# Optimization experiments

Measured on AMD Instinct MI355X. Metric: run time of the kernel, lower is better.

## Reference

```python
import jax, jax.numpy as jnp
import numpy as np

H = 2048      # hidden_size
I = 8192      # dense intermediate_size
MI = 1024     # moe_intermediate_size
E = 8         # num_local_experts
K = 2         # num_experts_per_tok
B, S = 2, 1024
EPS = 1e-6
ROOT = H ** (-0.5)


def _rms(x, w=None, eps=EPS):
    # fp32 RMSNorm matching _Gemma4CPURMSNorm; w=None -> no-scale variant
    ms = jnp.mean(x * x, axis=-1, keepdims=True) + eps
    y = x * jax.lax.rsqrt(ms)
    return y * w if w is not None else y


def _gelu_tanh(x):
    # gelu_pytorch_tanh == tanh-approximate gelu
    return jax.nn.gelu(x, approximate=True)


def setup_inputs() -> dict:
    key = jax.random.key(0)
    ks = jax.random.split(key, 10)
    s = 0.02
    return {
        "hidden_states": jax.random.normal(ks[0], (B, S, H), jnp.float32),
        # RMSNorm scales (init ones, as in nn.Parameter(torch.ones(dim)))
        "rn_pre1": jnp.ones((H,), jnp.float32),
        "rn_pre2": jnp.ones((H,), jnp.float32),
        "rn_post1": jnp.ones((H,), jnp.float32),
        "rn_post2": jnp.ones((H,), jnp.float32),
        "rn_post": jnp.ones((H,), jnp.float32),
        # dense GLU MLP weights, stored (in, out)
        "w_gate": jax.random.normal(ks[1], (H, I), jnp.float32) * s,
        "w_up":   jax.random.normal(ks[2], (H, I), jnp.float32) * s,
        "w_down": jax.random.normal(ks[3], (I, H), jnp.float32) * s,
        # router
        "router_w": jax.random.normal(ks[4], (H, E), jnp.float32) * s,
        "router_scale": jnp.ones((H,), jnp.float32),
        "per_expert_scale": jnp.ones((E,), jnp.float32),
        # per-expert GLU weights, stacked over experts
        "we_gate": jax.random.normal(ks[5], (E, H, MI), jnp.float32) * s,
        "we_up":   jax.random.normal(ks[6], (E, H, MI), jnp.float32) * s,
        "we_down": jax.random.normal(ks[7], (E, MI, H), jnp.float32) * s,
    }


def reference(hidden_states, rn_pre1, rn_pre2, rn_post1, rn_post2, rn_post,
              w_gate, w_up, w_down, router_w, router_scale, per_expert_scale,
              we_gate, we_up, we_down):
    b, s, h = hidden_states.shape
    T = b * s

    # --- dense branch ---
    dense_in = _rms(hidden_states, rn_pre1)                      # (B,S,H)
    dense_out = (_gelu_tanh(dense_in @ w_gate) * (dense_in @ w_up)) @ w_down
    dense_out = _rms(dense_out, rn_post1)                        # (B,S,H)

    # --- router (takes the raw residual, applies its own no-scale RMSNorm) ---
    x = hidden_states.reshape(T, h)
    xr = _rms(x) * router_scale * ROOT                           # (T,H)
    router_logits = xr @ router_w                                # (T,E)
    probs = jax.nn.softmax(router_logits, axis=-1)
    top_w, top_i = jax.lax.top_k(probs, K)                       # (T,K)
    top_w = top_w / jnp.sum(top_w, axis=-1, keepdims=True)
    top_w = top_w * per_expert_scale[top_i]
    aff = jnp.zeros((T, E), x.dtype).at[jnp.arange(T)[:, None], top_i].set(top_w)

    # --- MoE experts (compute all experts, combine with sparse affinities) ---
    moe_in = _rms(hidden_states, rn_pre2).reshape(T, h)          # (T,H)
    g = jnp.einsum('th,ehm->tem', moe_in, we_gate)               # (T,E,MI)
    u = jnp.einsum('th,ehm->tem', moe_in, we_up)
    eo = jnp.einsum('tem,emh->teh', _gelu_tanh(g) * u, we_down)  # (T,E,H)
    moe_out = jnp.einsum('te,teh->th', aff, eo).reshape(b, s, h)
    moe_out = _rms(moe_out, rn_post2)

    return _rms(dense_out + moe_out, rn_post)
```

## Files before the change

### kernel.cpp

```cpp
#include <hip/hip_runtime.h>
#include <stdint.h>

#define TOK 2048
#define HD  2048
#define ID  8192
#define MID 1024
#define NE  8
#define KSPLIT 4

typedef __attribute__((ext_vector_type(8))) short s16x8;
typedef __attribute__((ext_vector_type(4))) short s16x4;
typedef __attribute__((ext_vector_type(4))) float f32x4;

constexpr float EPSF  = 1e-6f;
constexpr float ROOTF = 0.02209708691207961f;

#define MFMA(a, b, c) __builtin_amdgcn_mfma_f32_16x16x32_bf16(a, b, c, 0, 0, 0)
#define BAR() __builtin_amdgcn_s_barrier()
#define SCHED0() __builtin_amdgcn_sched_barrier(0)
#define VMCNT(n) asm volatile("s_waitcnt vmcnt(" #n ")" ::: "memory")

__device__ __forceinline__ void gload16(const void* g, void* l) {
  __builtin_amdgcn_global_load_lds(
      (const __attribute__((address_space(1))) void*)g,
      (__attribute__((address_space(3))) void*)l, 16, 0, 0);
}

__device__ __forceinline__ short f2bf(float f) {
  union { float f; uint32_t u; } v; v.f = f;
  uint32_t r = v.u + 0x7fffu + ((v.u >> 16) & 1u);
  return (short)(r >> 16);
}

__device__ __forceinline__ float bf2f(short s) {
  union { uint32_t u; float f; } v; v.u = ((uint32_t)(uint16_t)s) << 16;
  return v.f;
}

__device__ __forceinline__ float gelu_tanh(float x) {
  float x3 = x * x * x;
  float u = 0.7978845608028654f * (x + 0.044715f * x3);
  return 0.5f * x * (1.0f + tanhf(u));
}

__global__ __launch_bounds__(256) void k_rms_router(
    const float* __restrict__ x, const float* __restrict__ rnp1,
    const float* __restrict__ rnp2, const float* __restrict__ rsc,
    const float* __restrict__ rw, const float* __restrict__ pes,
    short* __restrict__ rms1, short* __restrict__ rms2,
    int* __restrict__ cnt, int* __restrict__ tokl,
    float* __restrict__ wgtl, int* __restrict__ slotl) {
  const int t = blockIdx.x, tid = threadIdx.x;
  const size_t base = (size_t)t * HD;
  f32x4 v[2];
  float ss = 0.f;
#pragma unroll
  for (int i = 0; i < 2; ++i) {
    v[i] = *(const f32x4*)(x + base + tid * 4 + i * 1024);
#pragma unroll
    for (int j = 0; j < 4; ++j) ss += v[i][j] * v[i][j];
  }
  __shared__ float sr[4];
  __shared__ float sl[32];
#pragma unroll
  for (int off = 32; off; off >>= 1) ss += __shfl_down(ss, off, 64);
  if ((tid & 63) == 0) sr[tid >> 6] = ss;
  __syncthreads();
  const float inv = rsqrtf((sr[0] + sr[1] + sr[2] + sr[3]) * (1.0f / HD) + EPSF);
  float p[8] = {0, 0, 0, 0, 0, 0, 0, 0};
#pragma unroll
  for (int i = 0; i < 2; ++i) {
    const int h = tid * 4 + i * 1024;
    f32x4 w1 = *(const f32x4*)(rnp1 + h);
    f32x4 w2 = *(const f32x4*)(rnp2 + h);
    f32x4 sc = *(const f32x4*)(rsc + h);
    s16x4 o1, o2;
#pragma unroll
    for (int j = 0; j < 4; ++j) {
      float xn = v[i][j] * inv;
      o1[j] = f2bf(xn * w1[j]);
      o2[j] = f2bf(xn * w2[j]);
      float xq = xn * sc[j] * ROOTF;
      const float* rr = rw + (size_t)(h + j) * NE;
      f32x4 ra = *(const f32x4*)rr;
      f32x4 rb = *(const f32x4*)(rr + 4);
      p[0] += xq * ra[0]; p[1] += xq * ra[1]; p[2] += xq * ra[2]; p[3] += xq * ra[3];
      p[4] += xq * rb[0]; p[5] += xq * rb[1]; p[6] += xq * rb[2]; p[7] += xq * rb[3];
    }
    *(s16x4*)(rms1 + base + h) = o1;
    *(s16x4*)(rms2 + base + h) = o2;
  }
#pragma unroll
  for (int e = 0; e < 8; ++e)
#pragma unroll
    for (int off = 32; off; off >>= 1) p[e] += __shfl_down(p[e], off, 64);
  if ((tid & 63) == 0) {
#pragma unroll
    for (int e = 0; e < 8; ++e) sl[(tid >> 6) * 8 + e] = p[e];
  }
  __syncthreads();
  if (tid == 0) {
    float l[8];
#pragma unroll
    for (int e = 0; e < 8; ++e) l[e] = sl[e] + sl[8 + e] + sl[16 + e] + sl[24 + e];
    int i1 = 0;
#pragma unroll
    for (int e = 1; e < 8; ++e) if (l[e] > l[i1]) i1 = e;
    int i2 = (i1 == 0) ? 1 : 0;
#pragma unroll
    for (int e = 0; e < 8; ++e) if (e != i1 && l[e] > l[i2]) i2 = e;
    float p2 = expf(l[i2] - l[i1]);
    float s = 1.0f + p2;
    float w1 = (1.0f / s) * pes[i1];
    float w2 = (p2 / s) * pes[i2];
    int q1 = atomicAdd(&cnt[i1], 1);
    tokl[i1 * TOK + q1] = t; wgtl[i1 * TOK + q1] = w1; slotl[i1 * TOK + q1] = 0;
    int q2 = atomicAdd(&cnt[i2], 1);
    tokl[i2 * TOK + q2] = t; wgtl[i2 * TOK + q2] = w2; slotl[i2 * TOK + q2] = 1;
  }
}

__global__ __launch_bounds__(256) void k_transpose(
    const float* __restrict__ in, short* __restrict__ out, int R, int C) {
  __shared__ float tile[64 * 65];
  const int tid = threadIdx.x;
  const int c0 = blockIdx.x * 64, r0 = blockIdx.y * 64;
  const size_t bo = (size_t)blockIdx.z * R * C;
#pragma unroll
  for (int i = 0; i < 4; ++i) {
    int idx = tid + 256 * i;
    int r = idx >> 4, c4 = idx & 15;
    f32x4 f = *(const f32x4*)(in + bo + (size_t)(r0 + r) * C + c0 + c4 * 4);
#pragma unroll
    for (int j = 0; j < 4; ++j) tile[(c4 * 4 + j) * 65 + r] = f[j];
  }
  __syncthreads();
#pragma unroll
  for (int i = 0; i < 2; ++i) {
    int ch = tid + 256 * i;
    int c = ch >> 3, rs = ch & 7;
    s16x8 o;
#pragma unroll
    for (int q = 0; q < 8; ++q) o[q] = f2bf(tile[c * 65 + rs * 8 + q]);
    *(s16x8*)(out + bo + (size_t)(c0 + c) * R + r0 + rs * 8) = o;
  }
}

__global__ __launch_bounds__(512, 2) void k_gemm256(
    const short* __restrict__ Wt,
    const short* __restrict__ X,
    short* __restrict__ C) {
  __shared__ char lds[2][65536];
  const int tid = threadIdx.x;
  const int lane = tid & 63, wave = tid >> 6;
  const int wr = wave >> 2, wc = wave & 3;
  const int ln15 = lane & 15, l16 = lane >> 4;
  const int m0 = blockIdx.x * 256, t0 = blockIdx.y * 256;
  const int swz = (ln15 & 7) << 4;
  const int srow = tid >> 3;
  const int sslot = ((tid & 7) ^ ((tid >> 3) & 7)) << 4;
  const char* Wb = (const char*)Wt;
  const char* Xb = (const char*)X;
  auto STAGE = [&](int kt, int s) {
#pragma unroll
    for (int c = 0; c < 4; ++c) {
      gload16(Wb + (size_t)(m0 + c * 64 + srow) * 4096 + kt * 128 + sslot,
              &lds[s][c * 8192] + wave * 1024);
      gload16(Xb + (size_t)(t0 + c * 64 + srow) * 4096 + kt * 128 + sslot,
              &lds[s][32768 + c * 8192] + wave * 1024);
    }
  };
  f32x4 acc[8][4];
#pragma unroll
  for (int m = 0; m < 8; ++m)
#pragma unroll
    for (int n = 0; n < 4; ++n) acc[m][n] = (f32x4)0.f;
  const int NT = HD / 64;
  STAGE(0, 0);
  STAGE(1, 1);
  VMCNT(8);
  SCHED0();
  BAR();
#pragma unroll 2
  for (int kt = 0; kt < NT; ++kt) {
    const int s = kt & 1;
    const char* sA = &lds[s][0];
    const char* sB = &lds[s][32768];
#pragma unroll
    for (int mh = 0; mh < 2; ++mh)
#pragma unroll
      for (int ks = 0; ks < 2; ++ks) {
        const int ka = (ks * 64 + l16 * 16) ^ swz;
        s16x8 a[4], b[4];
#pragma unroll
        for (int f = 0; f < 4; ++f)
          a[f] = *(const s16x8*)(sA + (wr * 128 + mh * 64 + f * 16 + ln15) * 128 + ka);
#pragma unroll
        for (int n = 0; n < 4; ++n)
          b[n] = *(const s16x8*)(sB + (wc * 64 + n * 16 + ln15) * 128 + ka);
        __builtin_amdgcn_s_setprio(1);
#pragma unroll
        for (int f = 0; f < 4; ++f)
#pragma unroll
          for (int n = 0; n < 4; ++n)
            acc[mh * 4 + f][n] = MFMA(a[f], b[n], acc[mh * 4 + f][n]);
        __builtin_amdgcn_s_setprio(0);
      }
    BAR();
    if (kt + 2 < NT) {
      STAGE(kt + 2, s);
      VMCNT(8);
    } else if (kt + 1 < NT) {
      VMCNT(0);
    }
    SCHED0();
    BAR();
  }
#pragma unroll
  for (int mi = 0; mi < 8; ++mi)
#pragma unroll
    for (int n = 0; n < 4; ++n) {
      const int t = t0 + wc * 64 + n * 16 + ln15;
      const int i = m0 + wr * 128 + mi * 16 + l16 * 4;
      s16x4 o;
#pragma unroll
      for (int r = 0; r < 4; ++r) o[r] = f2bf(acc[mi][n][r]);
      *(s16x4*)(C + (size_t)t * ID + i) = o;
    }
}

__global__ __launch_bounds__(256) void k_gelumul(
    const short* __restrict__ g, const short* __restrict__ u,
    short* __restrict__ o) {
  const size_t idx = ((size_t)blockIdx.x * 256 + threadIdx.x) * 8;
  s16x8 gv = *(const s16x8*)(g + idx);
  s16x8 uv = *(const s16x8*)(u + idx);
  s16x8 ov;
#pragma unroll
  for (int j = 0; j < 8; ++j)
    ov[j] = f2bf(gelu_tanh(bf2f(gv[j])) * bf2f(uv[j]));
  *(s16x8*)(o + idx) = ov;
}

__global__ __launch_bounds__(256) void k_dense_down(
    const short* __restrict__ wdT,
    const short* __restrict__ act,
    float* __restrict__ dparts) {
  __shared__ short sW[128 * 32];
  __shared__ short sX[128 * 32];
  const int tid = threadIdx.x;
  const int n0 = blockIdx.x * 128, t0 = blockIdx.y * 128;
  const int kbase = blockIdx.z * (ID / KSPLIT);
  const int lane = tid & 63, wave = tid >> 6;
  const int wr = wave >> 1, wc = wave & 1;
  const int ln15 = lane & 15, k8 = (lane >> 4) * 8;
  const int srow = tid >> 2, skc = (tid & 3) * 8;
  const short* gW0 = wdT + (size_t)(n0 + srow) * ID + kbase + skc;
  const short* gW1 = wdT + (size_t)(n0 + 64 + srow) * ID + kbase + skc;
  const short* gX0 = act + (size_t)(t0 + srow) * ID + kbase + skc;
  const short* gX1 = act + (size_t)(t0 + 64 + srow) * ID + kbase + skc;
  char* lW = (char*)sW + wave * 1024;
  char* lX = (char*)sX + wave * 1024;
  f32x4 acc[4][4];
#pragma unroll
  for (int m = 0; m < 4; ++m)
#pragma unroll
    for (int n = 0; n < 4; ++n) acc[m][n] = (f32x4)0.f;
  for (int kt = 0; kt < ID / KSPLIT / 32; ++kt) {
    const int ko = kt * 32;
    __syncthreads();
    gload16(gW0 + ko, lW);
    gload16(gW1 + ko, lW + 4096);
    gload16(gX0 + ko, lX);
    gload16(gX1 + ko, lX + 4096);
    __syncthreads();
    s16x8 a[4], b[4];
#pragma unroll
    for (int m = 0; m < 4; ++m)
      a[m] = *(const s16x8*)(sW + (wr * 64 + m * 16 + ln15) * 32 + k8);
#pragma unroll
    for (int n = 0; n < 4; ++n)
      b[n] = *(const s16x8*)(sX + (wc * 64 + n * 16 + ln15) * 32 + k8);
#pragma unroll
    for (int m = 0; m < 4; ++m)
#pragma unroll
      for (int n = 0; n < 4; ++n) acc[m][n] = MFMA(a[m], b[n], acc[m][n]);
  }
  float* dst = dparts + (size_t)blockIdx.z * TOK * HD;
#pragma unroll
  for (int n = 0; n < 4; ++n) {
    const int t = t0 + wc * 64 + n * 16 + ln15;
#pragma unroll
    for (int m = 0; m < 4; ++m) {
      const int h = n0 + wr * 64 + m * 16 + (lane >> 4) * 4;
      *(f32x4*)(dst + (size_t)t * HD + h) = acc[m][n];
    }
  }
}

__global__ __launch_bounds__(256) void k_exp_gateup(
    const short* __restrict__ wegT, const short* __restrict__ weuT,
    const short* __restrict__ rms2,
    const int* __restrict__ cnt, const int* __restrict__ tokl,
    short* __restrict__ acte) {
  const int e = blockIdx.z;
  const int cn = cnt[e];
  const int t0 = blockIdx.y * 128;
  if (t0 >= cn) return;
  const int n0 = blockIdx.x * 64;
  __shared__ short sW[128 * 32];
  __shared__ short sX[128 * 32];
  const int tid = threadIdx.x;
  const int lane = tid & 63, wave = tid >> 6;
  const int ln15 = lane & 15, k8 = (lane >> 4) * 8;
  const int nsub = (wave & 1) * 32, tsub = (wave >> 1) * 64;
  const int srow = tid >> 2, skc = (tid & 3) * 8;
  const int* tl = tokl + e * TOK;
  int r0 = t0 + srow, r1 = t0 + 64 + srow;
  int tk0 = tl[r0 < cn ? r0 : cn - 1];
  int tk1 = tl[r1 < cn ? r1 : cn - 1];
  const short* gW0 = wegT + (size_t)e * MID * HD + (size_t)(n0 + srow) * HD + skc;
  const short* gW1 = weuT + (size_t)e * MID * HD + (size_t)(n0 + srow) * HD + skc;
  const short* gX0 = rms2 + (size_t)tk0 * HD + skc;
  const short* gX1 = rms2 + (size_t)tk1 * HD + skc;
  char* lW = (char*)sW + wave * 1024;
  char* lX = (char*)sX + wave * 1024;
  f32x4 accg[2][4], accu[2][4];
#pragma unroll
  for (int m = 0; m < 2; ++m)
#pragma unroll
    for (int n = 0; n < 4; ++n) { accg[m][n] = (f32x4)0.f; accu[m][n] = (f32x4)0.f; }
  for (int kt = 0; kt < HD / 32; ++kt) {
    const int ko = kt * 32;
    __syncthreads();
    gload16(gW0 + ko, lW);
    gload16(gW1 + ko, lW + 4096);
    gload16(gX0 + ko, lX);
    gload16(gX1 + ko, lX + 4096);
    __syncthreads();
    s16x8 ag[2], au[2], bx[4];
#pragma unroll
    for (int m = 0; m < 2; ++m) {
      ag[m] = *(const s16x8*)(sW + (nsub + m * 16 + ln15) * 32 + k8);
      au[m] = *(const s16x8*)(sW + (64 + nsub + m * 16 + ln15) * 32 + k8);
    }
#pragma unroll
    for (int n = 0; n < 4; ++n)
      bx[n] = *(const s16x8*)(sX + (tsub + n * 16 + ln15) * 32 + k8);
#pragma unroll
    for (int m = 0; m < 2; ++m)
#pragma unroll
      for (int n = 0; n < 4; ++n) {
        accg[m][n] = MFMA(ag[m], bx[n], accg[m][n]);
        accu[m][n] = MFMA(au[m], bx[n], accu[m][n]);
      }
  }
#pragma unroll
  for (int m = 0; m < 2; ++m)
#pragma unroll
    for (int n = 0; n < 4; ++n) {
      const int r = t0 + tsub + n * 16 + ln15;
      if (r < cn) {
        const int ib = n0 + nsub + m * 16 + (lane >> 4) * 4;
        s16x4 o;
#pragma unroll
        for (int q = 0; q < 4; ++q)
          o[q] = f2bf(gelu_tanh(accg[m][n][q]) * accu[m][n][q]);
        *(s16x4*)(acte + (size_t)e * TOK * MID + (size_t)r * MID + ib) = o;
      }
    }
}

__global__ __launch_bounds__(256) void k_exp_down(
    const short* __restrict__ wedT,
    const short* __restrict__ acte,
    const int* __restrict__ cnt, const int* __restrict__ tokl,
    const float* __restrict__ wgtl, const int* __restrict__ slotl,
    float* __restrict__ moep) {
  const int e = blockIdx.z;
  const int cn = cnt[e];
  const int t0 = blockIdx.y * 128;
  if (t0 >= cn) return;
  const int n0 = blockIdx.x * 128;
  __shared__ short sW[128 * 32];
  __shared__ short sX[128 * 32];
  const int tid = threadIdx.x;
  const int lane = tid & 63, wave = tid >> 6;
  const int wr = wave >> 1, wc = wave & 1;
  const int ln15 = lane & 15, k8 = (lane >> 4) * 8;
  const int srow = tid >> 2, skc = (tid & 3) * 8;
  const short* wb = wedT + (size_t)e * HD * MID;
  const short* gW0 = wb + (size_t)(n0 + srow) * MID + skc;
  const short* gW1 = wb + (size_t)(n0 + 64 + srow) * MID + skc;
  const short* ab = acte + (size_t)e * TOK * MID;
  const short* gX0 = ab + (size_t)(t0 + srow) * MID + skc;
  const short* gX1 = ab + (size_t)(t0 + 64 + srow) * MID + skc;
  char* lW = (char*)sW + wave * 1024;
  char* lX = (char*)sX + wave * 1024;
  f32x4 acc[4][4];
#pragma unroll
  for (int m = 0; m < 4; ++m)
#pragma unroll
    for (int n = 0; n < 4; ++n) acc[m][n] = (f32x4)0.f;
  for (int kt = 0; kt < MID / 32; ++kt) {
    const int ko = kt * 32;
    __syncthreads();
    gload16(gW0 + ko, lW);
    gload16(gW1 + ko, lW + 4096);
    gload16(gX0 + ko, lX);
    gload16(gX1 + ko, lX + 4096);
    __syncthreads();
    s16x8 a[4], b[4];
#pragma unroll
    for (int m = 0; m < 4; ++m)
      a[m] = *(const s16x8*)(sW + (wr * 64 + m * 16 + ln15) * 32 + k8);
#pragma unroll
    for (int n = 0; n < 4; ++n)
      b[n] = *(const s16x8*)(sX + (wc * 64 + n * 16 + ln15) * 32 + k8);
#pragma unroll
    for (int m = 0; m < 4; ++m)
#pragma unroll
      for (int n = 0; n < 4; ++n) acc[m][n] = MFMA(a[m], b[n], acc[m][n]);
  }
#pragma unroll
  for (int n = 0; n < 4; ++n) {
    const int r = t0 + wc * 64 + n * 16 + ln15;
    if (r < cn) {
      const int tk = tokl[e * TOK + r];
      const float wf = wgtl[e * TOK + r];
      const int sl = slotl[e * TOK + r];
      float* dst = moep + (size_t)sl * TOK * HD + (size_t)tk * HD;
#pragma unroll
      for (int m = 0; m < 4; ++m) {
        const int h = n0 + wr * 64 + m * 16 + (lane >> 4) * 4;
        f32x4 v = acc[m][n] * wf;
        *(f32x4*)(dst + h) = v;
      }
    }
  }
}

__global__ __launch_bounds__(256) void k_final(
    const float* __restrict__ dparts, const float* __restrict__ moep,
    const float* __restrict__ rno1, const float* __restrict__ rno2,
    const float* __restrict__ rnof, float* __restrict__ out) {
  const int t = blockIdx.x, tid = threadIdx.x;
  const size_t base = (size_t)t * HD;
  f32x4 dv[2], mv[2];
  float ssd = 0.f, ssm = 0.f;
#pragma unroll
  for (int i = 0; i < 2; ++i) {
    const int h = tid * 4 + i * 1024;
    dv[i] = (f32x4)0.f;
#pragma unroll
    for (int z = 0; z < KSPLIT; ++z)
      dv[i] += *(const f32x4*)(dparts + (size_t)z * TOK * HD + base + h);
    f32x4 a = *(const f32x4*)(moep + base + h);
    f32x4 b = *(const f32x4*)(moep + (size_t)TOK * HD + base + h);
    mv[i] = a + b;
#pragma unroll
    for (int j = 0; j < 4; ++j) { ssd += dv[i][j] * dv[i][j]; ssm += mv[i][j] * mv[i][j]; }
  }
  __shared__ float sr[8];
#pragma unroll
  for (int off = 32; off; off >>= 1) {
    ssd += __shfl_down(ssd, off, 64);
    ssm += __shfl_down(ssm, off, 64);
  }
  if ((tid & 63) == 0) { sr[tid >> 6] = ssd; sr[4 + (tid >> 6)] = ssm; }
  __syncthreads();
  const float invd = rsqrtf((sr[0] + sr[1] + sr[2] + sr[3]) * (1.0f / HD) + EPSF);
  const float invm = rsqrtf((sr[4] + sr[5] + sr[6] + sr[7]) * (1.0f / HD) + EPSF);
  f32x4 y[2];
  float ssy = 0.f;
#pragma unroll
  for (int i = 0; i < 2; ++i) {
    const int h = tid * 4 + i * 1024;
    f32x4 w1 = *(const f32x4*)(rno1 + h);
    f32x4 w2 = *(const f32x4*)(rno2 + h);
#pragma unroll
    for (int j = 0; j < 4; ++j) {
      y[i][j] = dv[i][j] * invd * w1[j] + mv[i][j] * invm * w2[j];
      ssy += y[i][j] * y[i][j];
    }
  }
  __syncthreads();
#pragma unroll
  for (int off = 32; off; off >>= 1) ssy += __shfl_down(ssy, off, 64);
  if ((tid & 63) == 0) sr[tid >> 6] = ssy;
  __syncthreads();
  const float invy = rsqrtf((sr[0] + sr[1] + sr[2] + sr[3]) * (1.0f / HD) + EPSF);
#pragma unroll
  for (int i = 0; i < 2; ++i) {
    const int h = tid * 4 + i * 1024;
    f32x4 w = *(const f32x4*)(rnof + h);
    f32x4 o;
#pragma unroll
    for (int j = 0; j < 4; ++j) o[j] = y[i][j] * invy * w[j];
    *(f32x4*)(out + base + h) = o;
  }
}

extern "C" void kernel_launch(void* const* d_in, const int* in_sizes, int n_in,
                              void* d_out, int out_size, void* d_ws, size_t ws_size,
                              hipStream_t stream) {
  (void)in_sizes; (void)n_in; (void)out_size;
  const float* x    = (const float*)d_in[0];
  const float* rnp1 = (const float*)d_in[1];
  const float* rnp2 = (const float*)d_in[2];
  const float* rno1 = (const float*)d_in[3];
  const float* rno2 = (const float*)d_in[4];
  const float* rnof = (const float*)d_in[5];
  const float* wg   = (const float*)d_in[6];
  const float* wu   = (const float*)d_in[7];
  const float* wd   = (const float*)d_in[8];
  const float* rw   = (const float*)d_in[9];
  const float* rsc  = (const float*)d_in[10];
  const float* pes  = (const float*)d_in[11];
  const float* weg  = (const float*)d_in[12];
  const float* weu  = (const float*)d_in[13];
  const float* wed  = (const float*)d_in[14];
  float* out = (float*)d_out;

  char* ws = (char*)d_ws;
  size_t off = 0;
  auto alloc = [&](size_t bytes) -> void* {
    void* p = ws + off;
    off += (bytes + 255) & ~(size_t)255;
    return p;
  };
  const size_t IH  = (size_t)ID * HD;
  const size_t EMH = (size_t)NE * MID * HD;
  short* wgT   = (short*)alloc(IH * 2);
  short* wuT   = (short*)alloc(IH * 2);
  short* wdT   = (short*)alloc(IH * 2);
  short* wegT  = (short*)alloc(EMH * 2);
  short* weuT  = (short*)alloc(EMH * 2);
  short* wedT  = (short*)alloc(EMH * 2);
  short* rms1  = (short*)alloc((size_t)TOK * HD * 2);
  short* rms2  = (short*)alloc((size_t)TOK * HD * 2);
  short* actb  = (short*)alloc((size_t)TOK * ID * 2);
  short* acte  = (short*)alloc((size_t)NE * TOK * MID * 2);
  float* moep  = (float*)alloc((size_t)2 * TOK * HD * 4);
  int*   cnt   = (int*)alloc(NE * 4);
  int*   tokl  = (int*)alloc((size_t)NE * TOK * 4);
  float* wgtl  = (float*)alloc((size_t)NE * TOK * 4);
  int*   slotl = (int*)alloc((size_t)NE * TOK * 4);
  if (off > ws_size) return;
  float* dparts = (float*)wgT;
  short* gbuf = acte;
  short* ubuf = (short*)moep;

  hipMemsetAsync(cnt, 0, NE * 4, stream);
  k_rms_router<<<TOK, 256, 0, stream>>>(x, rnp1, rnp2, rsc, rw, pes,
                                        rms1, rms2, cnt, tokl, wgtl, slotl);
  k_transpose<<<dim3(ID / 64, HD / 64, 1), 256, 0, stream>>>(wg, wgT, HD, ID);
  k_transpose<<<dim3(ID / 64, HD / 64, 1), 256, 0, stream>>>(wu, wuT, HD, ID);
  k_transpose<<<dim3(HD / 64, ID / 64, 1), 256, 0, stream>>>(wd, wdT, ID, HD);
  k_transpose<<<dim3(MID / 64, HD / 64, NE), 256, 0, stream>>>(weg, wegT, HD, MID);
  k_transpose<<<dim3(MID / 64, HD / 64, NE), 256, 0, stream>>>(weu, weuT, HD, MID);
  k_transpose<<<dim3(HD / 64, MID / 64, NE), 256, 0, stream>>>(wed, wedT, MID, HD);
  k_gemm256<<<dim3(ID / 256, TOK / 256), 512, 0, stream>>>(wgT, rms1, gbuf);
  k_gemm256<<<dim3(ID / 256, TOK / 256), 512, 0, stream>>>(wuT, rms1, ubuf);
  k_gelumul<<<(TOK * (size_t)ID) / (256 * 8), 256, 0, stream>>>(gbuf, ubuf, actb);
  k_dense_down<<<dim3(HD / 128, TOK / 128, KSPLIT), 256, 0, stream>>>(wdT, actb, dparts);
  k_exp_gateup<<<dim3(MID / 64, TOK / 128, NE), 256, 0, stream>>>(wegT, weuT, rms2,
                                                                  cnt, tokl, acte);
  k_exp_down<<<dim3(HD / 128, TOK / 128, NE), 256, 0, stream>>>(wedT, acte, cnt, tokl,
                                                                wgtl, slotl, moep);
  k_final<<<TOK, 256, 0, stream>>>(dparts, moep, rno1, rno2, rnof, out);
}
```

Measured before the change: 613.7 us.

## Fuse dense gate/up GEMMs and replace dense-down with pipelined 256x256 tile kernel

```diff
diff --git a/kernel.cpp b/kernel.cpp
--- a/kernel.cpp
+++ b/kernel.cpp
@@ -4,6 +4,7 @@
 #define TOK 2048
 #define HD  2048
 #define ID  8192
+#define ID2 16384
 #define MID 1024
 #define NE  8
 #define KSPLIT 4
@@ -225,77 +226,105 @@
       s16x4 o;
 #pragma unroll
       for (int r = 0; r < 4; ++r) o[r] = f2bf(acc[mi][n][r]);
-      *(s16x4*)(C + (size_t)t * ID + i) = o;
+      *(s16x4*)(C + (size_t)t * ID2 + i) = o;
+    }
+}
+
+__global__ __launch_bounds__(512, 2) void k_dd256(
+    const short* __restrict__ Wd,
+    const short* __restrict__ X,
+    float* __restrict__ dparts) {
+  __shared__ char lds[2][65536];
+  const int tid = threadIdx.x;
+  const int lane = tid & 63, wave = tid >> 6;
+  const int wr = wave >> 2, wc = wave & 3;
+  const int ln15 = lane & 15, l16 = lane >> 4;
+  const int m0 = blockIdx.x * 256, t0 = blockIdx.y * 256;
+  const size_t kB = (size_t)blockIdx.z * 4096;
+  const int swz = (ln15 & 7) << 4;
+  const int srow = tid >> 3;
+  const int sslot = ((tid & 7) ^ ((tid >> 3) & 7)) << 4;
+  const char* Wb = (const char*)Wd;
+  const char* Xb = (const char*)X;
+  auto STAGE = [&](int kt, int s) {
+#pragma unroll
+    for (int c = 0; c < 4; ++c) {
+      gload16(Wb + (size_t)(m0 + c * 64 + srow) * 16384 + kB + kt * 128 + sslot,
+              &lds[s][c * 8192] + wave * 1024);
+      gload16(Xb + (size_t)(t0 + c * 64 + srow) * 16384 + kB + kt * 128 + sslot,
+              &lds[s][32768 + c * 8192] + wave * 1024);
+    }
+  };
+  f32x4 acc[8][4];
+#pragma unroll
+  for (int m = 0; m < 8; ++m)
+#pragma unroll
+    for (int n = 0; n < 4; ++n) acc[m][n] = (f32x4)0.f;
+  const int NT = (ID / KSPLIT) / 64;
+  STAGE(0, 0);
+  STAGE(1, 1);
+  VMCNT(8);
+  SCHED0();
+  BAR();
+#pragma unroll 2
+  for (int kt = 0; kt < NT; ++kt) {
+    const int s = kt & 1;
+    const char* sA = &lds[s][0];
+    const char* sB = &lds[s][32768];
+#pragma unroll
+    for (int mh = 0; mh < 2; ++mh)
+#pragma unroll
+      for (int ks = 0; ks < 2; ++ks) {
+        const int ka = (ks * 64 + l16 * 16) ^ swz;
+        s16x8 a[4], b[4];
+#pragma unroll
+        for (int f = 0; f < 4; ++f)
+          a[f] = *(const s16x8*)(sA + (wr * 128 + mh * 64 + f * 16 + ln15) * 128 + ka);
+#pragma unroll
+        for (int n = 0; n < 4; ++n)
+          b[n] = *(const s16x8*)(sB + (wc * 64 + n * 16 + ln15) * 128 + ka);
+        __builtin_amdgcn_s_setprio(1);
+#pragma unroll
+        for (int f = 0; f < 4; ++f)
+#pragma unroll
+          for (int n = 0; n < 4; ++n)
+            acc[mh * 4 + f][n] = MFMA(a[f], b[n], acc[mh * 4 + f][n]);
+        __builtin_amdgcn_s_setprio(0);
+      }
+    BAR();
+    if (kt + 2 < NT) {
+      STAGE(kt + 2, s);
+      VMCNT(8);
+    } else if (kt + 1 < NT) {
+      VMCNT(0);
+    }
+    SCHED0();
+    BAR();
+  }
+  float* dst = dparts + (size_t)blockIdx.z * TOK * HD;
+#pragma unroll
+  for (int mi = 0; mi < 8; ++mi)
+#pragma unroll
+    for (int n = 0; n < 4; ++n) {
+      const int t = t0 + wc * 64 + n * 16 + ln15;
+      const int h = m0 + wr * 128 + mi * 16 + l16 * 4;
+      *(f32x4*)(dst + (size_t)t * HD + h) = acc[mi][n];
     }
 }
 
 __global__ __launch_bounds__(256) void k_gelumul(
-    const short* __restrict__ g, const short* __restrict__ u,
-    short* __restrict__ o) {
-  const size_t idx = ((size_t)blockIdx.x * 256 + threadIdx.x) * 8;
-  s16x8 gv = *(const s16x8*)(g + idx);
-  s16x8 uv = *(const s16x8*)(u + idx);
+    const short* __restrict__ cbuf, short* __restrict__ o) {
+  const int flat = blockIdx.x * 256 + threadIdx.x;
+  const int t = flat >> 10;
+  const int i8 = (flat & 1023) * 8;
+  const short* g = cbuf + (size_t)t * ID2 + i8;
+  s16x8 gv = *(const s16x8*)g;
+  s16x8 uv = *(const s16x8*)(g + ID);
   s16x8 ov;
 #pragma unroll
   for (int j = 0; j < 8; ++j)
     ov[j] = f2bf(gelu_tanh(bf2f(gv[j])) * bf2f(uv[j]));
-  *(s16x8*)(o + idx) = ov;
-}
-
-__global__ __launch_bounds__(256) void k_dense_down(
-    const short* __restrict__ wdT,
-    const short* __restrict__ act,
-    float* __restrict__ dparts) {
-  __shared__ short sW[128 * 32];
-  __shared__ short sX[128 * 32];
-  const int tid = threadIdx.x;
-  const int n0 = blockIdx.x * 128, t0 = blockIdx.y * 128;
-  const int kbase = blockIdx.z * (ID / KSPLIT);
-  const int lane = tid & 63, wave = tid >> 6;
-  const int wr = wave >> 1, wc = wave & 1;
-  const int ln15 = lane & 15, k8 = (lane >> 4) * 8;
-  const int srow = tid >> 2, skc = (tid & 3) * 8;
-  const short* gW0 = wdT + (size_t)(n0 + srow) * ID + kbase + skc;
-  const short* gW1 = wdT + (size_t)(n0 + 64 + srow) * ID + kbase + skc;
-  const short* gX0 = act + (size_t)(t0 + srow) * ID + kbase + skc;
-  const short* gX1 = act + (size_t)(t0 + 64 + srow) * ID + kbase + skc;
-  char* lW = (char*)sW + wave * 1024;
-  char* lX = (char*)sX + wave * 1024;
-  f32x4 acc[4][4];
-#pragma unroll
-  for (int m = 0; m < 4; ++m)
-#pragma unroll
-    for (int n = 0; n < 4; ++n) acc[m][n] = (f32x4)0.f;
-  for (int kt = 0; kt < ID / KSPLIT / 32; ++kt) {
-    const int ko = kt * 32;
-    __syncthreads();
-    gload16(gW0 + ko, lW);
-    gload16(gW1 + ko, lW + 4096);
-    gload16(gX0 + ko, lX);
-    gload16(gX1 + ko, lX + 4096);
-    __syncthreads();
-    s16x8 a[4], b[4];
-#pragma unroll
-    for (int m = 0; m < 4; ++m)
-      a[m] = *(const s16x8*)(sW + (wr * 64 + m * 16 + ln15) * 32 + k8);
-#pragma unroll
-    for (int n = 0; n < 4; ++n)
-      b[n] = *(const s16x8*)(sX + (wc * 64 + n * 16 + ln15) * 32 + k8);
-#pragma unroll
-    for (int m = 0; m < 4; ++m)
-#pragma unroll
-      for (int n = 0; n < 4; ++n) acc[m][n] = MFMA(a[m], b[n], acc[m][n]);
-  }
-  float* dst = dparts + (size_t)blockIdx.z * TOK * HD;
-#pragma unroll
-  for (int n = 0; n < 4; ++n) {
-    const int t = t0 + wc * 64 + n * 16 + ln15;
-#pragma unroll
-    for (int m = 0; m < 4; ++m) {
-      const int h = n0 + wr * 64 + m * 16 + (lane >> 4) * 4;
-      *(f32x4*)(dst + (size_t)t * HD + h) = acc[m][n];
-    }
-  }
+  *(s16x8*)(o + (size_t)t * ID + i8) = ov;
 }
 
 __global__ __launch_bounds__(256) void k_exp_gateup(
@@ -548,8 +577,7 @@
   int*   slotl = (int*)alloc((size_t)NE * TOK * 4);
   if (off > ws_size) return;
   float* dparts = (float*)wgT;
-  short* gbuf = acte;
-  short* ubuf = (short*)moep;
+  short* cbuf = acte;
 
   hipMemsetAsync(cnt, 0, NE * 4, stream);
   k_rms_router<<<TOK, 256, 0, stream>>>(x, rnp1, rnp2, rsc, rw, pes,
@@ -560,10 +588,9 @@
   k_transpose<<<dim3(MID / 64, HD / 64, NE), 256, 0, stream>>>(weg, wegT, HD, MID);
   k_transpose<<<dim3(MID / 64, HD / 64, NE), 256, 0, stream>>>(weu, weuT, HD, MID);
   k_transpose<<<dim3(HD / 64, MID / 64, NE), 256, 0, stream>>>(wed, wedT, MID, HD);
-  k_gemm256<<<dim3(ID / 256, TOK / 256), 512, 0, stream>>>(wgT, rms1, gbuf);
-  k_gemm256<<<dim3(ID / 256, TOK / 256), 512, 0, stream>>>(wuT, rms1, ubuf);
-  k_gelumul<<<(TOK * (size_t)ID) / (256 * 8), 256, 0, stream>>>(gbuf, ubuf, actb);
-  k_dense_down<<<dim3(HD / 128, TOK / 128, KSPLIT), 256, 0, stream>>>(wdT, actb, dparts);
+  k_gemm256<<<dim3(ID2 / 256, TOK / 256), 512, 0, stream>>>(wgT, rms1, cbuf);
+  k_gelumul<<<(TOK * ID) / (256 * 8), 256, 0, stream>>>(cbuf, actb);
+  k_dd256<<<dim3(HD / 256, TOK / 256, KSPLIT), 512, 0, stream>>>(wdT, actb, dparts);
   k_exp_gateup<<<dim3(MID / 64, TOK / 128, NE), 256, 0, stream>>>(wegT, weuT, rms2,
                                                                   cnt, tokl, acte);
   k_exp_down<<<dim3(HD / 128, TOK / 128, NE), 256, 0, stream>>>(wedT, acte, cnt, tokl,
```

Result: faster. 551.5 us (-10.1%).
